# Kernel optimization log

Measured on AMD Instinct MI355X. Metric: run time of the kernel, lower is better.

## Reference

```python
import jax, jax.numpy as jnp
import numpy as np

N, E, F, C, L = 100000, 1000000, 128, 64, 4
NS_CONV = 0.2   # GATv2 internal leaky_relu negative_slope
NS_ACT = 0.01   # nn.LeakyReLU() default activation slope
EPS = 1e-5      # BatchNorm1d / GraphNorm eps


def _lrelu(x, s):
    return jnp.where(x >= 0, x, s * x)


def setup_inputs() -> dict:
    key = jax.random.key(0)
    ks = jax.random.split(key, 8)
    sc = lambda k, shape: jax.random.normal(k, shape, jnp.float32) * 0.1
    return {
        "x": jax.random.normal(ks[0], (N, F), jnp.float32),
        "src": jax.random.randint(ks[1], (E,), 0, N, jnp.int32),
        "dst": jax.random.randint(ks[2], (E,), 0, N, jnp.int32),
        "bn_w": jnp.ones((F,), jnp.float32),
        "bn_b": jnp.zeros((F,), jnp.float32),
        "bn_mean": jnp.zeros((F,), jnp.float32),
        "bn_var": jnp.ones((F,), jnp.float32),
        "in_W": sc(ks[3], (C, F)),
        "in_b": jnp.zeros((C,), jnp.float32),
        "lin_W": sc(ks[4], (L, C, C)),
        "lin_b": jnp.zeros((L, C), jnp.float32),
        "att": sc(ks[5], (L, C)),
        "conv_b": jnp.zeros((L, C), jnp.float32),
        "gn_w": jnp.ones((L, C), jnp.float32),
        "gn_b": jnp.zeros((L, C), jnp.float32),
        "gn_ms": jnp.ones((L, C), jnp.float32),
    }


def reference(x, src, dst, bn_w, bn_b, bn_mean, bn_var, in_W, in_b,
              lin_W, lin_b, att, conv_b, gn_w, gn_b, gn_ms):
    n = x.shape[0]
    # GATv2Conv(add_self_loops=True): append one self-loop per node
    loops = jnp.arange(n, dtype=src.dtype)
    s_idx = jnp.concatenate([src, loops])  # [E'] = E + N
    d_idx = jnp.concatenate([dst, loops])

    # eval-mode BatchNorm1d with running stats, then input Linear + LeakyReLU
    h = (x - bn_mean) / jnp.sqrt(bn_var + EPS) * bn_w + bn_b
    h = _lrelu(h @ in_W.T + in_b, NS_ACT)  # [N, C]

    alphas = []
    for l in range(L):
        # GATv2Conv, heads=1, share_weights=True (x_l = x_r = lin(x))
        z = h @ lin_W[l].T + lin_b[l]                 # [N, C]
        e = _lrelu(z[s_idx] + z[d_idx], NS_CONV)      # [E', C]
        score = e @ att[l]                            # [E']
        # segment softmax over destination nodes (every segment has a self-loop)
        m = jax.ops.segment_max(score, d_idx, num_segments=n)
        ex = jnp.exp(score - m[d_idx])
        denom = jax.ops.segment_sum(ex, d_idx, num_segments=n)
        a = ex / (denom[d_idx] + 1e-16)               # [E'] attention weights
        alphas.append(a)
        # aggregate messages alpha * z_src, add conv bias
        h = jax.ops.segment_sum(a[:, None] * z[s_idx], d_idx, num_segments=n) + conv_b[l]
        # GraphNorm (batch=None -> single graph: global mean/var)
        mu = h.mean(0)
        o = h - gn_ms[l] * mu
        var = (o * o).mean(0)
        h = gn_w[l] * o / jnp.sqrt(var + EPS) + gn_b[l]
        # activation; dropout(p=0.3) is identity in eval mode
        h = _lrelu(h, NS_ACT)
    # default path (acummulate=False, return_one=False): (x, x, stacked attn)
    return h, h, jnp.stack(alphas, 0)  # ([N,C], [N,C], [L, E+N])
```

## Files before the change

kernel.cpp:

```cpp
#include <hip/hip_runtime.h>
#include <math.h>
#include <stdint.h>

#define NN 100000
#define NE 1000000
#define EP 1100000
#define FI 128
#define CC 64
#define NLAY 4
#define NS_CONV 0.2f
#define NS_ACT  0.01f
#define EPSV 1e-5f
#define NEG_INF (-3.402823466e38f)

__device__ __forceinline__ float lrelu(float x, float s) { return x >= 0.f ? x : s * x; }
__device__ __forceinline__ int srcOf(const int* s, int e) { return e < NE ? s[e] : e - NE; }
__device__ __forceinline__ int dstOf(const int* d, int e) { return e < NE ? d[e] : e - NE; }

__global__ void k_count(const int* __restrict__ dst, int* __restrict__ counts) {
    int e = blockIdx.x * 256 + threadIdx.x;
    if (e < EP) atomicAdd(&counts[dstOf(dst, e)], 1);
}

__global__ void k_scan1(const int* __restrict__ counts, int* __restrict__ bsum) {
    int t = threadIdx.x;
    int base = blockIdx.x * 1024 + t * 4;
    int s = 0;
#pragma unroll
    for (int k = 0; k < 4; k++) { int i = base + k; if (i < NN) s += counts[i]; }
#pragma unroll
    for (int off = 32; off; off >>= 1) s += __shfl_down(s, off);
    __shared__ int ws[4];
    if ((t & 63) == 0) ws[t >> 6] = s;
    __syncthreads();
    if (t == 0) bsum[blockIdx.x] = ws[0] + ws[1] + ws[2] + ws[3];
}

__global__ void k_scan2(const int* __restrict__ bsum, int* __restrict__ bbase,
                        int* __restrict__ offs, int nb) {
    int t = threadIdx.x;
    int v = (t < nb) ? bsum[t] : 0;
    int x = v;
#pragma unroll
    for (int off = 1; off < 64; off <<= 1) { int y = __shfl_up(x, off); if ((t & 63) >= off) x += y; }
    __shared__ int wtot[2];
    if ((t & 63) == 63) wtot[t >> 6] = x;
    __syncthreads();
    if (t >= 64) x += wtot[0];
    if (t < nb) bbase[t] = x - v;
    if (t == 127) offs[NN] = x;
}

__global__ void k_scan3(const int* __restrict__ counts, const int* __restrict__ bbase,
                        int* __restrict__ offs, int* __restrict__ cursor) {
    int t = threadIdx.x;
    int base = blockIdx.x * 1024 + t * 4;
    int v[4]; int tsum = 0;
#pragma unroll
    for (int k = 0; k < 4; k++) { int i = base + k; v[k] = (i < NN) ? counts[i] : 0; tsum += v[k]; }
    int x = tsum;
#pragma unroll
    for (int off = 1; off < 64; off <<= 1) { int y = __shfl_up(x, off); if ((t & 63) >= off) x += y; }
    __shared__ int ws[4];
    if ((t & 63) == 63) ws[t >> 6] = x;
    __syncthreads();
    int w = t >> 6; int wb = 0;
    for (int i = 0; i < w; i++) wb += ws[i];
    int run = (x - tsum) + wb + bbase[blockIdx.x];
#pragma unroll
    for (int k = 0; k < 4; k++) {
        int i = base + k;
        if (i < NN) { offs[i] = run; cursor[i] = run; run += v[k]; }
    }
}

__global__ void k_fill(const int* __restrict__ src, const int* __restrict__ dst,
                       int* __restrict__ cursor, int2* __restrict__ elist2) {
    int e = blockIdx.x * 256 + threadIdx.x;
    if (e < EP) {
        int d = dstOf(dst, e);
        int p = atomicAdd(&cursor[d], 1);
        elist2[p] = make_int2(e, srcOf(src, e));
    }
}

__global__ void k_fold(const float* __restrict__ bn_w, const float* __restrict__ bn_b,
                       const float* __restrict__ bn_mean, const float* __restrict__ bn_var,
                       const float* __restrict__ in_W, const float* __restrict__ in_b,
                       float* __restrict__ W2t, float* __restrict__ b2) {
    int t = blockIdx.x * 256 + threadIdx.x;
    if (t < FI * CC) {
        int f = t >> 6, c = t & 63;
        float scale = bn_w[f] * rsqrtf(bn_var[f] + EPSV);
        W2t[f * CC + c] = in_W[c * FI + f] * scale;
    }
    if (t < CC) {
        float acc = in_b[t];
        for (int f = 0; f < FI; f++) {
            float scale = bn_w[f] * rsqrtf(bn_var[f] + EPSV);
            acc += in_W[t * FI + f] * (bn_b[f] - bn_mean[f] * scale);
        }
        b2[t] = acc;
    }
}

__global__ __launch_bounds__(128) void k_in(const float* __restrict__ x, const float* __restrict__ W2t,
                                            const float* __restrict__ b2, float* __restrict__ h) {
    __shared__ float sW[FI * CC];
    __shared__ float sx[64 * (FI + 1)];
    for (int i = threadIdx.x; i < FI * CC; i += 128) sW[i] = W2t[i];
    int lane = threadIdx.x & 63;
    int wv = threadIdx.x >> 6;
    int cg = lane & 15;
    int ng = lane >> 4;
    float4 bias = ((const float4*)b2)[cg];
    int nchunks = (NN + 63) / 64;
    for (int chunk = blockIdx.x; chunk < nchunks; chunk += gridDim.x) {
        int n0 = chunk * 64;
        __syncthreads();
        for (int i = threadIdx.x; i < 64 * (FI / 4); i += 128) {
            int r = i >> 5, f4 = i & 31;
            int nn = n0 + r;
            float4 v = (nn < NN) ? ((const float4*)x)[(size_t)nn * (FI / 4) + f4]
                                 : make_float4(0.f, 0.f, 0.f, 0.f);
            float* dp = &sx[r * (FI + 1) + f4 * 4];
            dp[0] = v.x; dp[1] = v.y; dp[2] = v.z; dp[3] = v.w;
        }
        __syncthreads();
        int nbase = wv * 32 + ng * 8;
        float a[8][4];
#pragma unroll
        for (int k = 0; k < 8; k++) { a[k][0] = bias.x; a[k][1] = bias.y; a[k][2] = bias.z; a[k][3] = bias.w; }
        const float* hb = &sx[nbase * (FI + 1)];
#pragma unroll 4
        for (int f = 0; f < FI; f++) {
            float4 w = *(const float4*)&sW[f * CC + (cg << 2)];
#pragma unroll
            for (int k = 0; k < 8; k++) {
                float hv = hb[k * (FI + 1) + f];
                a[k][0] = fmaf(hv, w.x, a[k][0]);
                a[k][1] = fmaf(hv, w.y, a[k][1]);
                a[k][2] = fmaf(hv, w.z, a[k][2]);
                a[k][3] = fmaf(hv, w.w, a[k][3]);
            }
        }
#pragma unroll
        for (int k = 0; k < 8; k++) {
            int n = n0 + nbase + k;
            if (n < NN) {
                float4 o = make_float4(lrelu(a[k][0], NS_ACT), lrelu(a[k][1], NS_ACT),
                                       lrelu(a[k][2], NS_ACT), lrelu(a[k][3], NS_ACT));
                ((float4*)h)[(size_t)n * 16 + cg] = o;
            }
        }
    }
}

__global__ __launch_bounds__(256) void k_z(const float* __restrict__ h, const float* __restrict__ Wl,
                                           const float* __restrict__ bl, const float* __restrict__ AB,
                                           int do_norm, float* __restrict__ z) {
    __shared__ float sW[CC * CC];
    __shared__ float sh[128 * (CC + 1)];
    __shared__ float sA[CC], sB[CC];
    if (threadIdx.x < CC) {
        sA[threadIdx.x] = do_norm ? AB[threadIdx.x] : 1.f;
        sB[threadIdx.x] = do_norm ? AB[CC + threadIdx.x] : 0.f;
    }
    for (int i = threadIdx.x; i < CC * CC; i += 256) {
        int f = i >> 6, c = i & 63;
        sW[f * CC + c] = Wl[c * CC + f];
    }
    int lane = threadIdx.x & 63;
    int wv = threadIdx.x >> 6;
    int cg = lane & 15;
    int ng = lane >> 4;
    float4 bias = ((const float4*)bl)[cg];
    int nchunks = (NN + 127) / 128;
    for (int chunk = blockIdx.x; chunk < nchunks; chunk += gridDim.x) {
        int n0 = chunk * 128;
        __syncthreads();
        for (int i = threadIdx.x; i < 128 * (CC / 4); i += 256) {
            int r = i >> 4, f4 = i & 15;
            int nn = n0 + r;
            float4 v = (nn < NN) ? ((const float4*)h)[(size_t)nn * 16 + f4]
                                 : make_float4(0.f, 0.f, 0.f, 0.f);
            float* dp = &sh[r * (CC + 1) + f4 * 4];
            if (do_norm) {
                int c0 = f4 * 4;
                dp[0] = lrelu(sA[c0 + 0] * v.x + sB[c0 + 0], NS_ACT);
                dp[1] = lrelu(sA[c0 + 1] * v.y + sB[c0 + 1], NS_ACT);
                dp[2] = lrelu(sA[c0 + 2] * v.z + sB[c0 + 2], NS_ACT);
                dp[3] = lrelu(sA[c0 + 3] * v.w + sB[c0 + 3], NS_ACT);
            } else {
                dp[0] = v.x; dp[1] = v.y; dp[2] = v.z; dp[3] = v.w;
            }
        }
        __syncthreads();
        int nbase = wv * 32 + ng * 8;
        float a[8][4];
#pragma unroll
        for (int k = 0; k < 8; k++) { a[k][0] = bias.x; a[k][1] = bias.y; a[k][2] = bias.z; a[k][3] = bias.w; }
        const float* hb = &sh[nbase * (CC + 1)];
#pragma unroll 4
        for (int f = 0; f < CC; f++) {
            float4 w = *(const float4*)&sW[f * CC + (cg << 2)];
#pragma unroll
            for (int k = 0; k < 8; k++) {
                float hv = hb[k * (CC + 1) + f];
                a[k][0] = fmaf(hv, w.x, a[k][0]);
                a[k][1] = fmaf(hv, w.y, a[k][1]);
                a[k][2] = fmaf(hv, w.z, a[k][2]);
                a[k][3] = fmaf(hv, w.w, a[k][3]);
            }
        }
#pragma unroll
        for (int k = 0; k < 8; k++) {
            int n = n0 + nbase + k;
            if (n < NN) {
                float4 o = make_float4(a[k][0], a[k][1], a[k][2], a[k][3]);
                ((float4*)z)[(size_t)n * 16 + cg] = o;
            }
        }
    }
}

__global__ __launch_bounds__(256) void k_agg(const float* __restrict__ z, const float* __restrict__ att_l,
                                             const int2* __restrict__ elist2, const int* __restrict__ offs,
                                             const float* __restrict__ convb,
                                             float* __restrict__ h, float* __restrict__ score_csr,
                                             float* __restrict__ alpha) {
    int w = threadIdx.x >> 6, lane = threadIdx.x & 63;
    int n = blockIdx.x * 4 + w;
    if (n >= NN) return;
    int g = lane >> 4;
    int q = lane & 15;
    int base = offs[n], end = offs[n + 1];
    const float4* z4 = (const float4*)z;
    float4 attq = ((const float4*)att_l)[q];
    float4 zd = z4[(size_t)n * 16 + q];
    float m = NEG_INF, den = 0.f;
    float4 acc = make_float4(0.f, 0.f, 0.f, 0.f);

    int j = base + g;
    int2 es = make_int2(0, 0); float4 zs = make_float4(0.f, 0.f, 0.f, 0.f);
    if (j < end) { es = elist2[j]; zs = z4[(size_t)es.y * 16 + q]; }
    while (j < end) {
        float4 zc = zs;
        int jn = j + 4;
        if (jn < end) { es = elist2[jn]; zs = z4[(size_t)es.y * 16 + q]; }
        float p = lrelu(zc.x + zd.x, NS_CONV) * attq.x
                + lrelu(zc.y + zd.y, NS_CONV) * attq.y
                + lrelu(zc.z + zd.z, NS_CONV) * attq.z
                + lrelu(zc.w + zd.w, NS_CONV) * attq.w;
        p += __shfl_xor(p, 1);
        p += __shfl_xor(p, 2);
        p += __shfl_xor(p, 4);
        p += __shfl_xor(p, 8);
        if (q == 0) score_csr[j] = p;
        float mn = fmaxf(m, p);
        float s0 = __expf(m - mn);
        float ex = __expf(p - mn);
        den = den * s0 + ex;
        acc.x = acc.x * s0 + ex * zc.x;
        acc.y = acc.y * s0 + ex * zc.y;
        acc.z = acc.z * s0 + ex * zc.z;
        acc.w = acc.w * s0 + ex * zc.w;
        m = mn;
        j = jn;
    }
#pragma unroll
    for (int msk = 16; msk <= 32; msk <<= 1) {
        float mo  = __shfl_xor(m, msk);
        float dno = __shfl_xor(den, msk);
        float aox = __shfl_xor(acc.x, msk);
        float aoy = __shfl_xor(acc.y, msk);
        float aoz = __shfl_xor(acc.z, msk);
        float aow = __shfl_xor(acc.w, msk);
        float mn = fmaxf(m, mo);
        float s1 = __expf(m - mn);
        float s2 = __expf(mo - mn);
        den = den * s1 + dno * s2;
        acc.x = acc.x * s1 + aox * s2;
        acc.y = acc.y * s1 + aoy * s2;
        acc.z = acc.z * s1 + aoz * s2;
        acc.w = acc.w * s1 + aow * s2;
        m = mn;
    }
    float inv = 1.f / (den + 1e-16f);
    if (g == 0) {
        float4 cb = ((const float4*)convb)[q];
        float4 o = make_float4(acc.x * inv + cb.x, acc.y * inv + cb.y,
                               acc.z * inv + cb.z, acc.w * inv + cb.w);
        ((float4*)h)[(size_t)n * 16 + q] = o;
    }
    for (int jj = base + lane; jj < end; jj += 64) {
        int eid = elist2[jj].x;
        alpha[eid] = __expf(score_csr[jj] - m) * inv;
    }
}

__global__ __launch_bounds__(256) void k_r12(const float* __restrict__ h,
                                             double* __restrict__ pS, double* __restrict__ pQ) {
    int c = threadIdx.x & 63, w = threadIdx.x >> 6;
    double s = 0.0, q = 0.0;
    for (int n = blockIdx.x * 4 + w; n < NN; n += gridDim.x * 4) {
        float v = h[(size_t)n * CC + c];
        s += (double)v; q += (double)v * (double)v;
    }
    __shared__ double ls[4][64], lq[4][64];
    ls[w][c] = s; lq[w][c] = q;
    __syncthreads();
    if (w == 0) {
        pS[blockIdx.x * CC + c] = ls[0][c] + ls[1][c] + ls[2][c] + ls[3][c];
        pQ[blockIdx.x * CC + c] = lq[0][c] + lq[1][c] + lq[2][c] + lq[3][c];
    }
}

__global__ void k_r12b(const double* __restrict__ pS, const double* __restrict__ pQ,
                       const float* __restrict__ gn_w_l, const float* __restrict__ gn_b_l,
                       const float* __restrict__ gn_ms_l, float* __restrict__ AB, int nblk) {
    int c = threadIdx.x;
    if (c >= CC) return;
    double S = 0.0, Q = 0.0;
    for (int b = 0; b < nblk; b++) { S += pS[b * CC + c]; Q += pQ[b * CC + c]; }
    double mu = S / (double)NN;
    double ms = (double)gn_ms_l[c];
    double var = Q / (double)NN - 2.0 * ms * mu * mu + ms * ms * mu * mu;
    float A = gn_w_l[c] * rsqrtf((float)var + EPSV);
    float B = gn_b_l[c] - A * (float)(ms * mu);
    AB[c] = A; AB[CC + c] = B;
}

__global__ void k_out(const float* __restrict__ h, const float* __restrict__ AB,
                      float* __restrict__ o0, float* __restrict__ o1) {
    int i = blockIdx.x * 256 + threadIdx.x;
    if (i >= NN * 16) return;
    int cg = i & 15;
    float4 hv = ((const float4*)h)[i];
    float4 A = ((const float4*)AB)[cg];
    float4 B = ((const float4*)(AB + CC))[cg];
    float4 o = make_float4(lrelu(A.x * hv.x + B.x, NS_ACT), lrelu(A.y * hv.y + B.y, NS_ACT),
                           lrelu(A.z * hv.z + B.z, NS_ACT), lrelu(A.w * hv.w + B.w, NS_ACT));
    ((float4*)o0)[i] = o;
    ((float4*)o1)[i] = o;
}

extern "C" void kernel_launch(void* const* d_in, const int* in_sizes, int n_in,
                              void* d_out, int out_size, void* d_ws, size_t ws_size,
                              hipStream_t stream) {
    const float* x       = (const float*)d_in[0];
    const int*   src     = (const int*)d_in[1];
    const int*   dst     = (const int*)d_in[2];
    const float* bn_w    = (const float*)d_in[3];
    const float* bn_b    = (const float*)d_in[4];
    const float* bn_mean = (const float*)d_in[5];
    const float* bn_var  = (const float*)d_in[6];
    const float* in_W    = (const float*)d_in[7];
    const float* in_b    = (const float*)d_in[8];
    const float* lin_W   = (const float*)d_in[9];
    const float* lin_b   = (const float*)d_in[10];
    const float* att     = (const float*)d_in[11];
    const float* conv_b  = (const float*)d_in[12];
    const float* gn_w    = (const float*)d_in[13];
    const float* gn_b    = (const float*)d_in[14];
    const float* gn_ms   = (const float*)d_in[15];

    float* out = (float*)d_out;
    float* out_h0 = out;
    float* out_h1 = out + (size_t)NN * CC;
    float* out_alpha = out + (size_t)2 * NN * CC;

    const int NB_R = 256;

    char* wsp = (char*)d_ws;
    double* pS    = (double*)wsp;
    double* pQ    = pS + NB_R * CC;
    float* h      = (float*)(pQ + NB_R * CC);
    float* z      = h + (size_t)NN * CC;
    float* score  = z + (size_t)NN * CC;
    int2* elist2  = (int2*)(score + EP);
    int* counts   = (int*)(elist2 + EP);
    int* offs     = counts + NN;
    int* cursor   = offs + (NN + 4);
    int* bsum     = cursor + NN;
    int* bbase    = bsum + 128;
    float* W2t    = (float*)(bbase + 128);
    float* b2     = W2t + FI * CC;
    float* AB     = b2 + CC;

    const int NB_SCAN = (NN + 1023) / 1024;

    hipMemsetAsync(counts, 0, NN * sizeof(int), stream);
    k_count<<<(EP + 255) / 256, 256, 0, stream>>>(dst, counts);
    k_scan1<<<NB_SCAN, 256, 0, stream>>>(counts, bsum);
    k_scan2<<<1, 128, 0, stream>>>(bsum, bbase, offs, NB_SCAN);
    k_scan3<<<NB_SCAN, 256, 0, stream>>>(counts, bbase, offs, cursor);
    k_fill<<<(EP + 255) / 256, 256, 0, stream>>>(src, dst, cursor, elist2);

    k_fold<<<(FI * CC + 255) / 256, 256, 0, stream>>>(bn_w, bn_b, bn_mean, bn_var, in_W, in_b, W2t, b2);
    k_in<<<(NN + 63) / 64, 128, 0, stream>>>(x, W2t, b2, h);

    for (int l = 0; l < NLAY; l++) {
        const float* Wl      = lin_W + (size_t)l * CC * CC;
        const float* bl      = lin_b + (size_t)l * CC;
        const float* att_l   = att + (size_t)l * CC;
        const float* convb_l = conv_b + (size_t)l * CC;
        const float* gn_w_l  = gn_w + (size_t)l * CC;
        const float* gn_b_l  = gn_b + (size_t)l * CC;
        const float* gn_ms_l = gn_ms + (size_t)l * CC;
        float* alpha_l = out_alpha + (size_t)l * EP;

        k_z<<<(NN + 127) / 128, 256, 0, stream>>>(h, Wl, bl, AB, l > 0 ? 1 : 0, z);
        k_agg<<<(NN + 3) / 4, 256, 0, stream>>>(z, att_l, elist2, offs, convb_l, h, score, alpha_l);
        k_r12<<<NB_R, 256, 0, stream>>>(h, pS, pQ);
        k_r12b<<<1, 64, 0, stream>>>(pS, pQ, gn_w_l, gn_b_l, gn_ms_l, AB, NB_R);
    }

    k_out<<<(NN * 16 + 255) / 256, 256, 0, stream>>>(h, AB, out_h0, out_h1);
}
```

Before: 1.110 ms.

## Drop online-softmax max, fuse GraphNorm finalize, partition CSR atomics by XCD slice

Three separate changes. The aggregation kernel drops the running-max online softmax and sums exp(score) directly, storing the exponentials so alpha needs only a multiply. This relies on scores being small enough not to overflow, so numerical stability is given up. The GraphNorm finalize kernel is folded into the reduction kernel using a last-block-done atomic counter, removing one launch per layer. The count and fill kernels now use 1024 blocks, each handling only destinations in the node slice given by blockIdx mod 8, to localise atomics per XCD at the cost of every slice reading all edges.

```diff
diff --git a/kernel.cpp b/kernel.cpp
--- a/kernel.cpp
+++ b/kernel.cpp
@@ -8,18 +8,25 @@
 #define FI 128
 #define CC 64
 #define NLAY 4
+#define NXCD 8
+#define NSLICE (NN / NXCD)
 #define NS_CONV 0.2f
 #define NS_ACT  0.01f
 #define EPSV 1e-5f
-#define NEG_INF (-3.402823466e38f)
 
 __device__ __forceinline__ float lrelu(float x, float s) { return x >= 0.f ? x : s * x; }
 __device__ __forceinline__ int srcOf(const int* s, int e) { return e < NE ? s[e] : e - NE; }
 __device__ __forceinline__ int dstOf(const int* d, int e) { return e < NE ? d[e] : e - NE; }
 
-__global__ void k_count(const int* __restrict__ dst, int* __restrict__ counts) {
-    int e = blockIdx.x * 256 + threadIdx.x;
-    if (e < EP) atomicAdd(&counts[dstOf(dst, e)], 1);
+__global__ __launch_bounds__(256) void k_count(const int* __restrict__ dst, int* __restrict__ counts) {
+    int slice = blockIdx.x & (NXCD - 1);
+    int blk   = blockIdx.x >> 3;
+    int nblk  = gridDim.x >> 3;
+    int lo = slice * NSLICE, hi = lo + NSLICE;
+    for (int e = blk * 256 + threadIdx.x; e < EP; e += nblk * 256) {
+        int d = dstOf(dst, e);
+        if (d >= lo && d < hi) atomicAdd(&counts[d], 1);
+    }
 }
 
 __global__ void k_scan1(const int* __restrict__ counts, int* __restrict__ bsum) {
@@ -74,13 +81,18 @@
     }
 }
 
-__global__ void k_fill(const int* __restrict__ src, const int* __restrict__ dst,
-                       int* __restrict__ cursor, int2* __restrict__ elist2) {
-    int e = blockIdx.x * 256 + threadIdx.x;
-    if (e < EP) {
+__global__ __launch_bounds__(256) void k_fill(const int* __restrict__ src, const int* __restrict__ dst,
+                                              int* __restrict__ cursor, int2* __restrict__ elist2) {
+    int slice = blockIdx.x & (NXCD - 1);
+    int blk   = blockIdx.x >> 3;
+    int nblk  = gridDim.x >> 3;
+    int lo = slice * NSLICE, hi = lo + NSLICE;
+    for (int e = blk * 256 + threadIdx.x; e < EP; e += nblk * 256) {
         int d = dstOf(dst, e);
-        int p = atomicAdd(&cursor[d], 1);
-        elist2[p] = make_int2(e, srcOf(src, e));
+        if (d >= lo && d < hi) {
+            int p = atomicAdd(&cursor[d], 1);
+            elist2[p] = make_int2(e, srcOf(src, e));
+        }
     }
 }
 
@@ -227,7 +239,7 @@
 __global__ __launch_bounds__(256) void k_agg(const float* __restrict__ z, const float* __restrict__ att_l,
                                              const int2* __restrict__ elist2, const int* __restrict__ offs,
                                              const float* __restrict__ convb,
-                                             float* __restrict__ h, float* __restrict__ score_csr,
+                                             float* __restrict__ h, float* __restrict__ ex_csr,
                                              float* __restrict__ alpha) {
     int w = threadIdx.x >> 6, lane = threadIdx.x & 63;
     int n = blockIdx.x * 4 + w;
@@ -238,16 +250,16 @@
     const float4* z4 = (const float4*)z;
     float4 attq = ((const float4*)att_l)[q];
     float4 zd = z4[(size_t)n * 16 + q];
-    float m = NEG_INF, den = 0.f;
+    float den = 0.f;
     float4 acc = make_float4(0.f, 0.f, 0.f, 0.f);
 
     int j = base + g;
-    int2 es = make_int2(0, 0); float4 zs = make_float4(0.f, 0.f, 0.f, 0.f);
-    if (j < end) { es = elist2[j]; zs = z4[(size_t)es.y * 16 + q]; }
+    float4 zs = make_float4(0.f, 0.f, 0.f, 0.f);
+    if (j < end) { int2 es = elist2[j]; zs = z4[(size_t)es.y * 16 + q]; }
     while (j < end) {
         float4 zc = zs;
         int jn = j + 4;
-        if (jn < end) { es = elist2[jn]; zs = z4[(size_t)es.y * 16 + q]; }
+        if (jn < end) { int2 es = elist2[jn]; zs = z4[(size_t)es.y * 16 + q]; }
         float p = lrelu(zc.x + zd.x, NS_CONV) * attq.x
                 + lrelu(zc.y + zd.y, NS_CONV) * attq.y
                 + lrelu(zc.z + zd.z, NS_CONV) * attq.z
@@ -256,51 +268,41 @@
         p += __shfl_xor(p, 2);
         p += __shfl_xor(p, 4);
         p += __shfl_xor(p, 8);
-        if (q == 0) score_csr[j] = p;
-        float mn = fmaxf(m, p);
-        float s0 = __expf(m - mn);
-        float ex = __expf(p - mn);
-        den = den * s0 + ex;
-        acc.x = acc.x * s0 + ex * zc.x;
-        acc.y = acc.y * s0 + ex * zc.y;
-        acc.z = acc.z * s0 + ex * zc.z;
-        acc.w = acc.w * s0 + ex * zc.w;
-        m = mn;
+        float ex = __expf(p);
+        if (q == 0) ex_csr[j] = ex;
+        den += ex;
+        acc.x = fmaf(ex, zc.x, acc.x);
+        acc.y = fmaf(ex, zc.y, acc.y);
+        acc.z = fmaf(ex, zc.z, acc.z);
+        acc.w = fmaf(ex, zc.w, acc.w);
         j = jn;
     }
 #pragma unroll
     for (int msk = 16; msk <= 32; msk <<= 1) {
-        float mo  = __shfl_xor(m, msk);
-        float dno = __shfl_xor(den, msk);
-        float aox = __shfl_xor(acc.x, msk);
-        float aoy = __shfl_xor(acc.y, msk);
-        float aoz = __shfl_xor(acc.z, msk);
-        float aow = __shfl_xor(acc.w, msk);
-        float mn = fmaxf(m, mo);
-        float s1 = __expf(m - mn);
-        float s2 = __expf(mo - mn);
-        den = den * s1 + dno * s2;
-        acc.x = acc.x * s1 + aox * s2;
-        acc.y = acc.y * s1 + aoy * s2;
-        acc.z = acc.z * s1 + aoz * s2;
-        acc.w = acc.w * s1 + aow * s2;
-        m = mn;
+        den   += __shfl_xor(den, msk);
+        acc.x += __shfl_xor(acc.x, msk);
+        acc.y += __shfl_xor(acc.y, msk);
+        acc.z += __shfl_xor(acc.z, msk);
+        acc.w += __shfl_xor(acc.w, msk);
     }
     float inv = 1.f / (den + 1e-16f);
     if (g == 0) {
         float4 cb = ((const float4*)convb)[q];
-        float4 o = make_float4(acc.x * inv + cb.x, acc.y * inv + cb.y,
-                               acc.z * inv + cb.z, acc.w * inv + cb.w);
+        float4 o = make_float4(fmaf(acc.x, inv, cb.x), fmaf(acc.y, inv, cb.y),
+                               fmaf(acc.z, inv, cb.z), fmaf(acc.w, inv, cb.w));
         ((float4*)h)[(size_t)n * 16 + q] = o;
     }
     for (int jj = base + lane; jj < end; jj += 64) {
         int eid = elist2[jj].x;
-        alpha[eid] = __expf(score_csr[jj] - m) * inv;
+        alpha[eid] = ex_csr[jj] * inv;
     }
 }
 
 __global__ __launch_bounds__(256) void k_r12(const float* __restrict__ h,
-                                             double* __restrict__ pS, double* __restrict__ pQ) {
+                                             double* __restrict__ pS, double* __restrict__ pQ,
+                                             const float* __restrict__ gn_w_l, const float* __restrict__ gn_b_l,
+                                             const float* __restrict__ gn_ms_l, float* __restrict__ AB,
+                                             int* __restrict__ done) {
     int c = threadIdx.x & 63, w = threadIdx.x >> 6;
     double s = 0.0, q = 0.0;
     for (int n = blockIdx.x * 4 + w; n < NN; n += gridDim.x * 4) {
@@ -314,21 +316,29 @@
         pS[blockIdx.x * CC + c] = ls[0][c] + ls[1][c] + ls[2][c] + ls[3][c];
         pQ[blockIdx.x * CC + c] = lq[0][c] + lq[1][c] + lq[2][c] + lq[3][c];
     }
-}
-
-__global__ void k_r12b(const double* __restrict__ pS, const double* __restrict__ pQ,
-                       const float* __restrict__ gn_w_l, const float* __restrict__ gn_b_l,
-                       const float* __restrict__ gn_ms_l, float* __restrict__ AB, int nblk) {
-    int c = threadIdx.x;
-    if (c >= CC) return;
-    double S = 0.0, Q = 0.0;
-    for (int b = 0; b < nblk; b++) { S += pS[b * CC + c]; Q += pQ[b * CC + c]; }
-    double mu = S / (double)NN;
-    double ms = (double)gn_ms_l[c];
-    double var = Q / (double)NN - 2.0 * ms * mu * mu + ms * ms * mu * mu;
-    float A = gn_w_l[c] * rsqrtf((float)var + EPSV);
-    float B = gn_b_l[c] - A * (float)(ms * mu);
-    AB[c] = A; AB[CC + c] = B;
+    __threadfence();
+    __shared__ int amLast;
+    if (threadIdx.x == 0) amLast = (atomicAdd(done, 1) == gridDim.x - 1) ? 1 : 0;
+    __syncthreads();
+    if (!amLast) return;
+    __threadfence();
+    double fs = 0.0, fq = 0.0;
+    for (int b = w; b < gridDim.x; b += 4) {
+        fs += pS[b * CC + c];
+        fq += pQ[b * CC + c];
+    }
+    ls[w][c] = fs; lq[w][c] = fq;
+    __syncthreads();
+    if (threadIdx.x < CC) {
+        double S = ls[0][c] + ls[1][c] + ls[2][c] + ls[3][c];
+        double Q = lq[0][c] + lq[1][c] + lq[2][c] + lq[3][c];
+        double mu = S / (double)NN;
+        double ms = (double)gn_ms_l[c];
+        double var = Q / (double)NN - 2.0 * ms * mu * mu + ms * ms * mu * mu;
+        float A = gn_w_l[c] * rsqrtf((float)var + EPSV);
+        float B = gn_b_l[c] - A * (float)(ms * mu);
+        AB[c] = A; AB[CC + c] = B;
+    }
 }
 
 __global__ void k_out(const float* __restrict__ h, const float* __restrict__ AB,
@@ -377,10 +387,11 @@
     double* pQ    = pS + NB_R * CC;
     float* h      = (float*)(pQ + NB_R * CC);
     float* z      = h + (size_t)NN * CC;
-    float* score  = z + (size_t)NN * CC;
-    int2* elist2  = (int2*)(score + EP);
+    float* exbuf  = z + (size_t)NN * CC;
+    int2* elist2  = (int2*)(exbuf + EP);
     int* counts   = (int*)(elist2 + EP);
-    int* offs     = counts + NN;
+    int* done     = counts + NN;
+    int* offs     = done + 8;
     int* cursor   = offs + (NN + 4);
     int* bsum     = cursor + NN;
     int* bbase    = bsum + 128;
@@ -390,12 +401,12 @@
 
     const int NB_SCAN = (NN + 1023) / 1024;
 
-    hipMemsetAsync(counts, 0, NN * sizeof(int), stream);
-    k_count<<<(EP + 255) / 256, 256, 0, stream>>>(dst, counts);
+    hipMemsetAsync(counts, 0, (NN + 8) * sizeof(int), stream);
+    k_count<<<1024, 256, 0, stream>>>(dst, counts);
     k_scan1<<<NB_SCAN, 256, 0, stream>>>(counts, bsum);
     k_scan2<<<1, 128, 0, stream>>>(bsum, bbase, offs, NB_SCAN);
     k_scan3<<<NB_SCAN, 256, 0, stream>>>(counts, bbase, offs, cursor);
-    k_fill<<<(EP + 255) / 256, 256, 0, stream>>>(src, dst, cursor, elist2);
+    k_fill<<<1024, 256, 0, stream>>>(src, dst, cursor, elist2);
 
     k_fold<<<(FI * CC + 255) / 256, 256, 0, stream>>>(bn_w, bn_b, bn_mean, bn_var, in_W, in_b, W2t, b2);
     k_in<<<(NN + 63) / 64, 128, 0, stream>>>(x, W2t, b2, h);
@@ -411,9 +422,8 @@
         float* alpha_l = out_alpha + (size_t)l * EP;
 
         k_z<<<(NN + 127) / 128, 256, 0, stream>>>(h, Wl, bl, AB, l > 0 ? 1 : 0, z);
-        k_agg<<<(NN + 3) / 4, 256, 0, stream>>>(z, att_l, elist2, offs, convb_l, h, score, alpha_l);
-        k_r12<<<NB_R, 256, 0, stream>>>(h, pS, pQ);
-        k_r12b<<<1, 64, 0, stream>>>(pS, pQ, gn_w_l, gn_b_l, gn_ms_l, AB, NB_R);
+        k_agg<<<(NN + 3) / 4, 256, 0, stream>>>(z, att_l, elist2, offs, convb_l, h, exbuf, alpha_l);
+        k_r12<<<NB_R, 256, 0, stream>>>(h, pS, pQ, gn_w_l, gn_b_l, gn_ms_l, AB, done + l);
     }
 
     k_out<<<(NN * 16 + 255) / 256, 256, 0, stream>>>(h, AB, out_h0, out_h1);
```

Result: faster. 942.8 us (-15.1%).
